# Optimization experiments

Measured on AMD Instinct MI355X. Metric: run time of the kernel, lower is better.

The kernel has to match this reference:

```python
import jax, jax.numpy as jnp
import numpy as np
import math

B, T, C = 2, 2048, 2048
NH = 16
HS = C // NH

def setup_inputs() -> dict:
    key = jax.random.key(0)
    k1, k2, k3 = jax.random.split(key, 3)
    x = jax.random.normal(k1, (B, T, C), dtype=jnp.float32)
    w_attn = jax.random.normal(k2, (3 * C, C), dtype=jnp.float32) * 0.02
    w_proj = jax.random.normal(k3, (C, C), dtype=jnp.float32) * 0.02
    return {"x": x, "w_attn": w_attn, "w_proj": w_proj}

def reference(x, w_attn, w_proj):
    Bx, Tx, Cx = x.shape
    # qkv projection: Linear(C, 3C), no bias
    qkv = jnp.einsum('btc,oc->bto', x, w_attn)  # [B,T,3C]
    q, k, v = jnp.split(qkv, 3, axis=-1)
    # reshape to heads: [B,T,H,hs]
    q = q.reshape(Bx, Tx, NH, HS)
    k = k.reshape(Bx, Tx, NH, HS)
    v = v.reshape(Bx, Tx, NH, HS)
    # scores [B,H,Tq,Tk]
    att = jnp.einsum('bqhd,bkhd->bhqk', q, k) * (1.0 / math.sqrt(HS))
    causal = jnp.tril(jnp.ones((Tx, Tx), dtype=bool))
    att = jnp.where(causal[None, None], att, -jnp.inf)
    att = jax.nn.softmax(att, axis=-1)
    # attn_dropout with p=0.0 is identity
    y = jnp.einsum('bhqk,bkhd->bqhd', att, v)
    y = y.reshape(Bx, Tx, Cx)
    return jnp.einsum('btc,oc->bto', y, w_proj)
```

## Files before the change

### kernel.cpp

```cpp
#include <hip/hip_runtime.h>

typedef __attribute__((ext_vector_type(8))) short short8;
typedef __attribute__((ext_vector_type(4))) float f32x4;
typedef unsigned short u16;

#define T_SEQ 2048
#define C_DIM 2048

static __device__ __forceinline__ u16 f2bf(float f){
  unsigned u = __float_as_uint(f);
  u = (u + 0x7fffu + ((u >> 16) & 1u)) >> 16;
  return (u16)u;
}

__global__ void cvt3_kernel(const float* __restrict__ x,
                            const float* __restrict__ wa,
                            const float* __restrict__ wp,
                            u16* __restrict__ xb, u16* __restrict__ wab,
                            u16* __restrict__ wpb){
  int idx = blockIdx.x * blockDim.x + threadIdx.x;
  int stride = gridDim.x * blockDim.x;
  for (int i = idx; i < 6291456; i += stride){
    const float* src; u16* dst; int j;
    if (i < 2097152){ src = x;  dst = xb;  j = i; }
    else if (i < 5242880){ src = wa; dst = wab; j = i - 2097152; }
    else { src = wp; dst = wpb; j = i - 5242880; }
    float4 v = ((const float4*)src)[j];
    ushort4 o;
    o.x = f2bf(v.x); o.y = f2bf(v.y); o.z = f2bf(v.z); o.w = f2bf(v.w);
    ((ushort4*)dst)[j] = o;
  }
}

__device__ __forceinline__ void gl_lds16(const void* g, void* l){
  __builtin_amdgcn_global_load_lds(
      (const __attribute__((address_space(1))) unsigned int*)g,
      (__attribute__((address_space(3))) unsigned int*)l,
      16, 0, 0);
}

template<int MODE, typename OUT>
__global__ __launch_bounds__(256, 2) void gemm256(const u16* __restrict__ A,
                                                  const u16* __restrict__ B,
                                                  OUT* __restrict__ C,
                                                  u16* __restrict__ VT,
                                                  int M, int N, int K){
  __shared__ __align__(16) u16 lA[2][128*64];
  __shared__ __align__(16) u16 lB[2][128*64];
  const int tid  = threadIdx.x;
  const int lane = tid & 63;
  const int r16  = lane & 15;
  const int g4   = lane >> 4;
  const int wave = tid >> 6;
  const int wm = wave >> 1, wn = wave & 1;

  const int nwg = gridDim.x * gridDim.y;
  const int idl = blockIdx.y * gridDim.x + blockIdx.x;
  const int wg  = (idl & 7) * (nwg >> 3) + (idl >> 3);
  const int bx  = wg / gridDim.y, by = wg % gridDim.y;
  const int m0 = by * 128, n0 = bx * 128;

  f32x4 acc[4][4] = {};
  const int nt = K >> 6;

  auto stA = [&](int b, int t){
    #pragma unroll
    for (int c=0;c<4;c++){
      const int row0 = wave*32 + c*8;
      const int row  = row0 + (lane>>3);
      const int cole = (((lane&7) ^ (row&7)) << 3);
      gl_lds16(&A[(size_t)(m0+row)*K + t*64 + cole], &lA[b][row0*64]);
    }
  };
  auto stB2 = [&](int b, int t, int half){
    #pragma unroll
    for (int c=0;c<2;c++){
      const int row0 = (wave>>1)*64 + half*32 + (wave&1)*16 + c*8;
      const int row  = row0 + (lane>>3);
      const int cole = (((lane&7) ^ (row&7)) << 3);
      gl_lds16(&B[(size_t)(n0+row)*K + t*64 + cole], &lB[b][row0*64]);
    }
  };
  auto rdA = [&](short8 (&af)[4][2], int b){
    #pragma unroll
    for (int i=0;i<4;i++){
      const int R = wm*64 + i*16 + r16;
      #pragma unroll
      for (int ks=0;ks<2;ks++)
        af[i][ks] = *(const short8*)&lA[b][R*64 + ((g4*8 + ks*32) ^ ((R&7)<<3))];
    }
  };
  auto rdB = [&](short8 (&bf)[2][2], int b, int half){
    #pragma unroll
    for (int j=0;j<2;j++){
      const int R = wn*64 + half*32 + j*16 + r16;
      #pragma unroll
      for (int ks=0;ks<2;ks++)
        bf[j][ks] = *(const short8*)&lB[b][R*64 + ((g4*8 + ks*32) ^ ((R&7)<<3))];
    }
  };

  stA(0,0); stB2(0,0,0); stB2(0,0,1);
  asm volatile("s_waitcnt vmcnt(2)" ::: "memory");
  __builtin_amdgcn_s_barrier();
  asm volatile("" ::: "memory");

  for (int t = 0; t < nt; ++t){
    const int cb = t & 1, nb = cb ^ 1;
    const bool more = (t + 1 < nt);
    short8 af[4][2], bf[2][2];

    rdA(af, cb); rdB(bf, cb, 0);
    if (more){
      stA(nb, t+1); stB2(nb, t+1, 0);
      asm volatile("s_waitcnt vmcnt(6)" ::: "memory");
    } else {
      asm volatile("s_waitcnt vmcnt(0)" ::: "memory");
    }
    __builtin_amdgcn_s_barrier();
    asm volatile("s_waitcnt lgkmcnt(0)" ::: "memory");
    __builtin_amdgcn_sched_barrier(0);
    __builtin_amdgcn_s_setprio(1);
    #pragma unroll
    for (int i=0;i<4;i++)
      #pragma unroll
      for (int j=0;j<2;j++)
        #pragma unroll
        for (int ks=0;ks<2;ks++)
          acc[i][j] = __builtin_amdgcn_mfma_f32_16x16x32_bf16(af[i][ks], bf[j][ks], acc[i][j], 0,0,0);
    __builtin_amdgcn_s_setprio(0);
    __builtin_amdgcn_s_barrier();
    asm volatile("" ::: "memory");

    rdB(bf, cb, 1);
    if (more){
      stB2(nb, t+1, 1);
      asm volatile("s_waitcnt vmcnt(2)" ::: "memory");
    }
    __builtin_amdgcn_s_barrier();
    asm volatile("s_waitcnt lgkmcnt(0)" ::: "memory");
    __builtin_amdgcn_sched_barrier(0);
    __builtin_amdgcn_s_setprio(1);
    #pragma unroll
    for (int i=0;i<4;i++)
      #pragma unroll
      for (int j=0;j<2;j++)
        #pragma unroll
        for (int ks=0;ks<2;ks++)
          acc[i][2+j] = __builtin_amdgcn_mfma_f32_16x16x32_bf16(af[i][ks], bf[j][ks], acc[i][2+j], 0,0,0);
    __builtin_amdgcn_s_setprio(0);
    __builtin_amdgcn_s_barrier();
    asm volatile("" ::: "memory");
  }

  if (MODE == 1 && n0 >= 4096){
    #pragma unroll
    for (int i=0;i<4;i++){
      const int m = m0 + wm*64 + i*16 + g4*4;
      const int bb = m >> 11, tt = m & 2047;
      #pragma unroll
      for (int j=0;j<4;j++){
        const int cv = n0 + wn*64 + j*16 + r16 - 4096;
        const int h = cv >> 7, dl = cv & 127;
        ushort4 pack;
        pack.x = f2bf(acc[i][j][0]); pack.y = f2bf(acc[i][j][1]);
        pack.z = f2bf(acc[i][j][2]); pack.w = f2bf(acc[i][j][3]);
        *(ushort4*)&VT[(size_t)((bb<<4) + h)*262144 + (size_t)dl*2048 + tt] = pack;
      }
    }
  } else {
    const int ldc = (MODE == 1) ? 4096 : N;
    #pragma unroll
    for (int i=0;i<4;i++){
      const int row = m0 + wm*64 + i*16 + g4*4;
      #pragma unroll
      for (int j=0;j<4;j++){
        const int col = n0 + wn*64 + j*16 + r16;
        #pragma unroll
        for (int r=0;r<4;r++){
          float v = acc[i][j][r];
          if constexpr (sizeof(OUT)==2) C[(size_t)(row+r)*ldc + col] = (OUT)f2bf(v);
          else                          C[(size_t)(row+r)*ldc + col] = (OUT)v;
        }
      }
    }
  }
}

__global__ __launch_bounds__(256) void attn_kernel(const u16* __restrict__ qk,
                                                   const u16* __restrict__ vt,
                                                   u16* __restrict__ y){
  __shared__ __align__(16) u16 Kl[2][64*128];
  __shared__ __align__(16) u16 Vl[2][128*64];
  __shared__ __align__(16) u16 Pl[4][32*64];

  const int tid = threadIdx.x, lane = tid & 63, wave = tid >> 6;
  const int r16 = lane & 15, g4 = lane >> 4;

  const int id = blockIdx.x;
  const int xk = id & 7,  kk = id >> 3;
  const int bh = 4*xk + (kk & 3);
  const int a  = kk >> 2;
  const int bq = 31 - a;

  const int bb = bh >> 4, h = bh & 15;
  const int qcol = h*128, kcol = 2048 + h*128;
  const u16* vhead = vt + (size_t)bh * 262144;
  const float scale = 0.08838834764831845f;

  short8 qf0[4], qf1[4];
  {
    const u16* qp0 = qk + (size_t)(bb*T_SEQ + a*64  + wave*16 + r16)*4096 + qcol;
    const u16* qp1 = qk + (size_t)(bb*T_SEQ + bq*64 + wave*16 + r16)*4096 + qcol;
    #pragma unroll
    for (int c=0;c<4;c++){
      qf0[c] = *(const short8*)&qp0[g4*8 + c*32];
      qf1[c] = *(const short8*)&qp1[g4*8 + c*32];
    }
  }

  float m0r[4], m1r[4], l0r[4], l1r[4];
  #pragma unroll
  for (int r=0;r<4;r++){ m0r[r] = -1e30f; m1r[r] = -1e30f; l0r[r] = 0.f; l1r[r] = 0.f; }
  f32x4 o0[8] = {}, o1[8] = {};

  const int nt = bq + 1;

  auto stage = [&](int sbuf, int t){
    const size_t kbase = (size_t)(bb*T_SEQ + t*64)*4096 + kcol;
    #pragma unroll
    for (int c=0;c<4;c++){
      const int row0 = wave*16 + c*4;
      const int row  = row0 + g4;
      gl_lds16(&qk[kbase + (size_t)row*4096 + ((r16*8) ^ ((row&7)<<3))],
               &Kl[sbuf][row0*128]);
    }
    const int t0 = t*64;
    #pragma unroll
    for (int c=0;c<4;c++){
      const int idx = wave*4 + c;
      const int d   = idx*8 + (lane>>3);
      const int j8  = (lane&7)*8;
      gl_lds16(&vhead[(size_t)d*2048 + t0 + (j8 ^ ((d&7)<<3))],
               &Vl[sbuf][idx*512]);
    }
  };

  stage(0, 0);
  int cur = 0;

  for (int t = 0; t < nt; ++t){
    __syncthreads();
    if (t + 1 < nt) stage(cur^1, t+1);
    const bool act0 = (t <= a);

    float s0m[4][4], s1m[4][4];
    #pragma unroll
    for (int cc=0;cc<4;cc++){
      const int krow = cc*16 + r16;
      const int sw = (krow & 7) << 3;
      short8 kf[4];
      #pragma unroll
      for (int dc=0;dc<4;dc++)
        kf[dc] = *(const short8*)&Kl[cur][krow*128 + ((g4*8 + dc*32) ^ sw)];
      {
        f32x4 sv = {0.f,0.f,0.f,0.f};
        #pragma unroll
        for (int dc=0;dc<4;dc++)
          sv = __builtin_amdgcn_mfma_f32_16x16x32_bf16(qf1[dc], kf[dc], sv, 0,0,0);
        #pragma unroll
        for (int rr=0;rr<4;rr++) s1m[cc][rr] = sv[rr] * scale;
      }
      if (act0){
        f32x4 sv = {0.f,0.f,0.f,0.f};
        #pragma unroll
        for (int dc=0;dc<4;dc++)
          sv = __builtin_amdgcn_mfma_f32_16x16x32_bf16(qf0[dc], kf[dc], sv, 0,0,0);
        #pragma unroll
        for (int rr=0;rr<4;rr++) s0m[cc][rr] = sv[rr] * scale;
      }
    }
    if (t == a){
      #pragma unroll
      for (int cc=0;cc<4;cc++){
        const int kvl = cc*16 + r16;
        #pragma unroll
        for (int rr=0;rr<4;rr++){
          const int qi = wave*16 + g4*4 + rr;
          if (kvl > qi) s0m[cc][rr] = -1e30f;
        }
      }
    }
    if (t == bq){
      #pragma unroll
      for (int cc=0;cc<4;cc++){
        const int kvl = cc*16 + r16;
        #pragma unroll
        for (int rr=0;rr<4;rr++){
          const int qi = wave*16 + g4*4 + rr;
          if (kvl > qi) s1m[cc][rr] = -1e30f;
        }
      }
    }

    float lm0[4], lm1[4];
    #pragma unroll
    for (int rr=0;rr<4;rr++)
      lm1[rr] = fmaxf(fmaxf(s1m[0][rr], s1m[1][rr]), fmaxf(s1m[2][rr], s1m[3][rr]));
    if (act0)
      #pragma unroll
      for (int rr=0;rr<4;rr++)
        lm0[rr] = fmaxf(fmaxf(s0m[0][rr], s0m[1][rr]), fmaxf(s0m[2][rr], s0m[3][rr]));
    bool need = false;
    #pragma unroll
    for (int rr=0;rr<4;rr++) need = need || (lm1[rr] > m1r[rr] + 8.f);
    if (act0)
      #pragma unroll
      for (int rr=0;rr<4;rr++) need = need || (lm0[rr] > m0r[rr] + 8.f);
    if (__any(need)){
      #pragma unroll
      for (int rr=0;rr<4;rr++){
        float pmv = lm1[rr];
        #pragma unroll
        for (int off=1; off<16; off<<=1) pmv = fmaxf(pmv, __shfl_xor(pmv, off, 64));
        const float mnew = fmaxf(m1r[rr], pmv);
        const float corr = __expf(m1r[rr] - mnew);
        m1r[rr] = mnew;
        l1r[rr] *= corr;
        #pragma unroll
        for (int n=0;n<8;n++) o1[n][rr] *= corr;
      }
      if (act0){
        #pragma unroll
        for (int rr=0;rr<4;rr++){
          float pmv = lm0[rr];
          #pragma unroll
          for (int off=1; off<16; off<<=1) pmv = fmaxf(pmv, __shfl_xor(pmv, off, 64));
          const float mnew = fmaxf(m0r[rr], pmv);
          const float corr = __expf(m0r[rr] - mnew);
          m0r[rr] = mnew;
          l0r[rr] *= corr;
          #pragma unroll
          for (int n=0;n<8;n++) o0[n][rr] *= corr;
        }
      }
    }
    #pragma unroll
    for (int rr=0;rr<4;rr++){
      float s0 = 0.f;
      #pragma unroll
      for (int cc=0;cc<4;cc++){
        const float p = __expf(s1m[cc][rr] - m1r[rr]);
        s1m[cc][rr] = p;
        s0 += p;
      }
      #pragma unroll
      for (int off=1; off<16; off<<=1) s0 += __shfl_xor(s0, off, 64);
      l1r[rr] += s0;
    }
    if (act0){
      #pragma unroll
      for (int rr=0;rr<4;rr++){
        float s0 = 0.f;
        #pragma unroll
        for (int cc=0;cc<4;cc++){
          const float p = __expf(s0m[cc][rr] - m0r[rr]);
          s0m[cc][rr] = p;
          s0 += p;
        }
        #pragma unroll
        for (int off=1; off<16; off<<=1) s0 += __shfl_xor(s0, off, 64);
        l0r[rr] += s0;
      }
    }

    #pragma unroll
    for (int cc=0;cc<4;cc++)
      #pragma unroll
      for (int rr=0;rr<4;rr++){
        const int qr = 16 + g4*4 + rr;
        Pl[wave][qr*64 + ((cc*16 + r16) ^ ((qr&7)<<3))] = f2bf(s1m[cc][rr]);
      }
    if (act0){
      #pragma unroll
      for (int cc=0;cc<4;cc++)
        #pragma unroll
        for (int rr=0;rr<4;rr++){
          const int qr = g4*4 + rr;
          Pl[wave][qr*64 + ((cc*16 + r16) ^ ((qr&7)<<3))] = f2bf(s0m[cc][rr]);
        }
    }
    asm volatile("s_waitcnt lgkmcnt(0)" ::: "memory");

    short8 pf0[2], pf1[2];
    {
      const int qr1 = 16 + r16;
      const int sw1 = (qr1 & 7) << 3;
      pf1[0] = *(const short8*)&Pl[wave][qr1*64 + ((g4*8)      ^ sw1)];
      pf1[1] = *(const short8*)&Pl[wave][qr1*64 + ((g4*8 + 32) ^ sw1)];
      if (act0){
        const int qr0 = r16;
        const int sw0 = (qr0 & 7) << 3;
        pf0[0] = *(const short8*)&Pl[wave][qr0*64 + ((g4*8)      ^ sw0)];
        pf0[1] = *(const short8*)&Pl[wave][qr0*64 + ((g4*8 + 32) ^ sw0)];
      }
    }
    #pragma unroll
    for (int n=0;n<8;n++){
      const int vr = n*16 + r16;
      const int sw = (vr & 7) << 3;
      short8 vf0 = *(const short8*)&Vl[cur][vr*64 + ((g4*8)      ^ sw)];
      short8 vf1 = *(const short8*)&Vl[cur][vr*64 + ((g4*8 + 32) ^ sw)];
      o1[n] = __builtin_amdgcn_mfma_f32_16x16x32_bf16(pf1[0], vf0, o1[n], 0,0,0);
      o1[n] = __builtin_amdgcn_mfma_f32_16x16x32_bf16(pf1[1], vf1, o1[n], 0,0,0);
      if (act0){
        o0[n] = __builtin_amdgcn_mfma_f32_16x16x32_bf16(pf0[0], vf0, o0[n], 0,0,0);
        o0[n] = __builtin_amdgcn_mfma_f32_16x16x32_bf16(pf0[1], vf1, o0[n], 0,0,0);
      }
    }
    cur ^= 1;
  }

  {
    const size_t yr0 = (size_t)(bb*T_SEQ + a*64 + wave*16 + g4*4) * C_DIM + h*128;
    #pragma unroll
    for (int n=0;n<8;n++)
      #pragma unroll
      for (int rr=0;rr<4;rr++){
        const float v = o0[n][rr] / l0r[rr];
        y[yr0 + (size_t)rr*C_DIM + n*16 + r16] = f2bf(v);
      }
  }
  {
    const size_t yr1 = (size_t)(bb*T_SEQ + bq*64 + wave*16 + g4*4) * C_DIM + h*128;
    #pragma unroll
    for (int n=0;n<8;n++)
      #pragma unroll
      for (int rr=0;rr<4;rr++){
        const float v = o1[n][rr] / l1r[rr];
        y[yr1 + (size_t)rr*C_DIM + n*16 + r16] = f2bf(v);
      }
  }
}

extern "C" void kernel_launch(void* const* d_in, const int* in_sizes, int n_in,
                              void* d_out, int out_size, void* d_ws, size_t ws_size,
                              hipStream_t stream){
  const float* x  = (const float*)d_in[0];
  const float* wa = (const float*)d_in[1];
  const float* wp = (const float*)d_in[2];
  float* out = (float*)d_out;

  u16* ws  = (u16*)d_ws;
  u16* xb  = ws;
  u16* wab = xb  + 8388608;
  u16* wpb = wab + 12582912;
  u16* qk  = wpb + 4194304;
  u16* vt  = qk  + 16777216;
  u16* yb  = xb;

  hipLaunchKernelGGL(cvt3_kernel, dim3(2048), dim3(256), 0, stream,
                     x, wa, wp, xb, wab, wpb);

  hipLaunchKernelGGL((gemm256<1,u16>),   dim3(48,32), dim3(256), 0, stream,
                     xb, wab, qk, vt, 4096, 6144, 2048);
  hipLaunchKernelGGL(attn_kernel,        dim3(512),  dim3(256), 0, stream,
                     qk, vt, yb);
  hipLaunchKernelGGL((gemm256<0,float>), dim3(16,32), dim3(256), 0, stream,
                     yb, wpb, out, (u16*)nullptr, 4096, 2048, 2048);
}
```

Before: 299.5 us.

## Load V fragments directly from global memory into registers, dropping LDS staging

```diff
diff --git a/kernel.cpp b/kernel.cpp
--- a/kernel.cpp
+++ b/kernel.cpp
@@ -191,7 +191,6 @@
                                                    const u16* __restrict__ vt,
                                                    u16* __restrict__ y){
   __shared__ __align__(16) u16 Kl[2][64*128];
-  __shared__ __align__(16) u16 Vl[2][128*64];
   __shared__ __align__(16) u16 Pl[4][32*64];
 
   const int tid = threadIdx.x, lane = tid & 63, wave = tid >> 6;
@@ -235,15 +234,6 @@
       gl_lds16(&qk[kbase + (size_t)row*4096 + ((r16*8) ^ ((row&7)<<3))],
                &Kl[sbuf][row0*128]);
     }
-    const int t0 = t*64;
-    #pragma unroll
-    for (int c=0;c<4;c++){
-      const int idx = wave*4 + c;
-      const int d   = idx*8 + (lane>>3);
-      const int j8  = (lane&7)*8;
-      gl_lds16(&vhead[(size_t)d*2048 + t0 + (j8 ^ ((d&7)<<3))],
-               &Vl[sbuf][idx*512]);
-    }
   };
 
   stage(0, 0);
@@ -253,6 +243,16 @@
     __syncthreads();
     if (t + 1 < nt) stage(cur^1, t+1);
     const bool act0 = (t <= a);
+
+    short8 vA[4][2];
+    {
+      const u16* vp0 = vhead + (size_t)r16*2048 + t*64 + g4*8;
+      #pragma unroll
+      for (int n=0;n<4;n++){
+        vA[n][0] = *(const short8*)(vp0 + (size_t)n*16*2048);
+        vA[n][1] = *(const short8*)(vp0 + (size_t)n*16*2048 + 32);
+      }
+    }
 
     float s0m[4][4], s1m[4][4];
     #pragma unroll
@@ -405,17 +405,32 @@
         pf0[1] = *(const short8*)&Pl[wave][qr0*64 + ((g4*8 + 32) ^ sw0)];
       }
     }
-    #pragma unroll
-    for (int n=0;n<8;n++){
-      const int vr = n*16 + r16;
-      const int sw = (vr & 7) << 3;
-      short8 vf0 = *(const short8*)&Vl[cur][vr*64 + ((g4*8)      ^ sw)];
-      short8 vf1 = *(const short8*)&Vl[cur][vr*64 + ((g4*8 + 32) ^ sw)];
-      o1[n] = __builtin_amdgcn_mfma_f32_16x16x32_bf16(pf1[0], vf0, o1[n], 0,0,0);
-      o1[n] = __builtin_amdgcn_mfma_f32_16x16x32_bf16(pf1[1], vf1, o1[n], 0,0,0);
+
+    short8 vB[4][2];
+    {
+      const u16* vp0 = vhead + (size_t)(64 + r16)*2048 + t*64 + g4*8;
+      #pragma unroll
+      for (int n=0;n<4;n++){
+        vB[n][0] = *(const short8*)(vp0 + (size_t)n*16*2048);
+        vB[n][1] = *(const short8*)(vp0 + (size_t)n*16*2048 + 32);
+      }
+    }
+    #pragma unroll
+    for (int n=0;n<4;n++){
+      o1[n] = __builtin_amdgcn_mfma_f32_16x16x32_bf16(pf1[0], vA[n][0], o1[n], 0,0,0);
+      o1[n] = __builtin_amdgcn_mfma_f32_16x16x32_bf16(pf1[1], vA[n][1], o1[n], 0,0,0);
       if (act0){
-        o0[n] = __builtin_amdgcn_mfma_f32_16x16x32_bf16(pf0[0], vf0, o0[n], 0,0,0);
-        o0[n] = __builtin_amdgcn_mfma_f32_16x16x32_bf16(pf0[1], vf1, o0[n], 0,0,0);
+        o0[n] = __builtin_amdgcn_mfma_f32_16x16x32_bf16(pf0[0], vA[n][0], o0[n], 0,0,0);
+        o0[n] = __builtin_amdgcn_mfma_f32_16x16x32_bf16(pf0[1], vA[n][1], o0[n], 0,0,0);
+      }
+    }
+    #pragma unroll
+    for (int n=0;n<4;n++){
+      o1[n+4] = __builtin_amdgcn_mfma_f32_16x16x32_bf16(pf1[0], vB[n][0], o1[n+4], 0,0,0);
+      o1[n+4] = __builtin_amdgcn_mfma_f32_16x16x32_bf16(pf1[1], vB[n][1], o1[n+4], 0,0,0);
+      if (act0){
+        o0[n+4] = __builtin_amdgcn_mfma_f32_16x16x32_bf16(pf0[0], vB[n][0], o0[n+4], 0,0,0);
+        o0[n+4] = __builtin_amdgcn_mfma_f32_16x16x32_bf16(pf0[1], vB[n][1], o0[n+4], 0,0,0);
       }
     }
     cur ^= 1;
```

Result: slower. 335.0 us (+11.8%).
